# Optimization experiments

Hardware: AMD Instinct MI355X
Metric: run time of the kernel (lower is better)

The kernel has to match this reference:

```python
import jax, jax.numpy as jnp
import numpy as np

NUM_HEADS = 12


def setup_inputs() -> dict:
    key = jax.random.key(0)
    k1, k2, k3 = jax.random.split(key, 3)
    B, N, C = 8, 1024, 768
    x = jax.random.normal(k1, (B, N, C), dtype=jnp.float32)
    qkv_w = jax.random.normal(k2, (3 * C, C), dtype=jnp.float32) * (C ** -0.5)
    proj_w = jax.random.normal(k3, (C, C), dtype=jnp.float32) * (C ** -0.5)
    proj_b = jnp.zeros((C,), dtype=jnp.float32)
    return {"x": x, "qkv_w": qkv_w, "proj_w": proj_w, "proj_b": proj_b, "cur_depth": 9}


def reference(x, qkv_w, proj_w, proj_b, cur_depth):
    B, N, C = x.shape
    H = NUM_HEADS
    hd = C // H
    scale = hd ** -0.5
    # qkv projection (no bias): (B,N,3C) -> (3,B,H,N,hd)
    qkv = (x @ qkv_w.T).reshape(B, N, 3, H, hd).transpose(2, 0, 3, 1, 4)
    q, k, v = qkv[0], qkv[1], qkv[2]
    # full attention scores, materialized as in the original
    attn = jnp.einsum("bhqd,bhkd->bhqk", q, k) * scale  # (B,H,N,N)
    # sigmoid gate from the LAST query row's pre-softmax scores, averaged over heads
    # attn[:, :, -1, :] -> (B,H,N); mean over heads -> (B,N); broadcast to (B,1,1,N)
    mask = jax.nn.sigmoid(attn[:, :, -1, :].mean(axis=1))[:, None, None, :]
    attn = jax.nn.softmax(attn, axis=-1)
    if cur_depth >= 9:
        attn = attn * mask
    out = jnp.einsum("bhqk,bhkd->bhqd", attn, v)  # (B,H,N,hd)
    out = out.transpose(0, 2, 1, 3).reshape(B, N, C)
    out = out @ proj_w.T + proj_b
    return (out, mask)
```

## Files before the change

### kernel.cpp

```cpp
#include <hip/hip_runtime.h>
#include <stdint.h>

typedef __bf16 bf16;
typedef __bf16 bf16x8 __attribute__((ext_vector_type(8)));
typedef float f32x4 __attribute__((ext_vector_type(4)));
typedef float f32x16 __attribute__((ext_vector_type(16)));
typedef uint32_t u32x4 __attribute__((ext_vector_type(4)));

#define DEVI static __device__ __forceinline__

DEVI void async_ld16(void* lds, const void* g) {
  __builtin_amdgcn_global_load_lds(
      (const __attribute__((address_space(1))) void*)(uintptr_t)g,
      (__attribute__((address_space(3))) void*)(uint32_t)(uintptr_t)lds,
      16, 0, 0);
}

DEVI f32x4 vsplat(float v) { f32x4 r; r.x = v; r.y = v; r.z = v; r.w = v; return r; }

__global__ __launch_bounds__(256) void cvt3_kernel(
    const float* __restrict__ x, bf16* __restrict__ xb,
    const float* __restrict__ w1, bf16* __restrict__ w1b,
    const float* __restrict__ w2, bf16* __restrict__ w2b) {
  int i = blockIdx.x * 256 + threadIdx.x;
  const float* src; bf16* dst; int idx;
  if (i < 786432) { src = x; dst = xb; idx = i; }
  else if (i < 786432 + 221184) { src = w1; dst = w1b; idx = i - 786432; }
  else if (i < 786432 + 221184 + 73728) { src = w2; dst = w2b; idx = i - 1007616; }
  else return;
  const float4* p = (const float4*)src + (size_t)idx * 2;
  float4 a = p[0], b = p[1];
  bf16x8 o;
  o[0] = (bf16)a.x; o[1] = (bf16)a.y; o[2] = (bf16)a.z; o[3] = (bf16)a.w;
  o[4] = (bf16)b.x; o[5] = (bf16)b.y; o[6] = (bf16)b.z; o[7] = (bf16)b.w;
  *((bf16x8*)dst + idx) = o;
}

DEVI void gemm_stage(bf16* AsD, bf16* BsD, const bf16* A, const bf16* B,
                     int K, int m0, int n0, int kt, int t, int wbase) {
#pragma unroll
  for (int i = 0; i < 2; i++) {
    int unit = i * 256 + t;
    int row = unit >> 2;
    int su = (unit & 3) ^ ((row >> 1) & 3);
    async_ld16(AsD + (size_t)(i * 256 + wbase) * 8,
               A + (size_t)(m0 + row) * K + kt + su * 8);
    async_ld16(BsD + (size_t)(i * 256 + wbase) * 8,
               B + (size_t)(n0 + row) * K + kt + su * 8);
  }
}

template <int MODE>
__global__ __launch_bounds__(256) void gemm_bt_kernel(
    const bf16* __restrict__ A, const bf16* __restrict__ B, int K, int N,
    int nx, bf16* __restrict__ q_out, bf16* __restrict__ k_out,
    bf16* __restrict__ vt_out, float* __restrict__ f_out,
    const float* __restrict__ bias) {
  __shared__ bf16 As[3][128 * 32];
  __shared__ bf16 Bs[3][128 * 32];
  const int t = threadIdx.x;
  const int lane = t & 63, g = lane >> 4, ql = lane & 15;
  const int w = t >> 6, wr = w >> 1, wc = w & 1;
  const int wbase = __builtin_amdgcn_readfirstlane(t & 192);
  const int bid = blockIdx.x;
  const int xcd = bid & 7, i6 = bid >> 3;
  const int yq = i6 / nx;
  const int m0 = (xcd * 8 + yq) * 128, n0 = (i6 - yq * nx) * 128;
  const int nk = K >> 5;

  f32x4 acc[4][4];
#pragma unroll
  for (int i = 0; i < 4; i++)
#pragma unroll
    for (int j = 0; j < 4; j++) acc[i][j] = vsplat(0.f);

  gemm_stage(As[0], Bs[0], A, B, K, m0, n0, 0, t, wbase);
  gemm_stage(As[1], Bs[1], A, B, K, m0, n0, 32, t, wbase);

  int rd = 0;
  for (int kt2 = 0; kt2 < nk; ++kt2) {
    if (kt2 + 1 < nk)
      asm volatile("s_waitcnt vmcnt(4)\n\ts_barrier" ::: "memory");
    else
      asm volatile("s_waitcnt vmcnt(0)\n\ts_barrier" ::: "memory");
    if (kt2 + 2 < nk) {
      int wb = rd >= 1 ? rd - 1 : 2;
      gemm_stage(As[wb], Bs[wb], A, B, K, m0, n0, (kt2 + 2) * 32, t, wbase);
    }
    const bf16* Asc = As[rd];
    const bf16* Bsc = Bs[rd];
    bf16x8 af[4], bfr[4];
#pragma unroll
    for (int f = 0; f < 4; f++) {
      int ra = wr * 64 + f * 16 + ql;
      af[f] = *(const bf16x8*)(Asc + ra * 32 + ((g ^ ((ra >> 1) & 3)) * 8));
      int rb = wc * 64 + f * 16 + ql;
      bfr[f] = *(const bf16x8*)(Bsc + rb * 32 + ((g ^ ((rb >> 1) & 3)) * 8));
    }
#pragma unroll
    for (int fm = 0; fm < 4; fm++)
#pragma unroll
      for (int fn = 0; fn < 4; fn++)
        acc[fm][fn] = __builtin_amdgcn_mfma_f32_16x16x32_bf16(af[fm], bfr[fn],
                                                              acc[fm][fn], 0, 0, 0);
    rd = rd < 2 ? rd + 1 : 0;
  }

  if (MODE == 0) {
#pragma unroll
    for (int fm = 0; fm < 4; fm++) {
#pragma unroll
      for (int fn = 0; fn < 4; fn++) {
        int n = n0 + wc * 64 + fn * 16 + ql;
#pragma unroll
        for (int r = 0; r < 4; r++) {
          int m = m0 + wr * 64 + fm * 16 + g * 4 + r;
          int b = m >> 10, nn = m & 1023;
          float v = acc[fm][fn][r];
          if (n < 768) {
            int h = n >> 6, d = n & 63;
            q_out[((size_t)((b * 12 + h) * 1024 + nn)) * 64 + d] = (bf16)(v * 0.125f);
          } else if (n < 1536) {
            int c = n - 768, h = c >> 6, d = c & 63;
            k_out[((size_t)((b * 12 + h) * 1024 + nn)) * 64 + d] = (bf16)v;
          } else {
            int c = n - 1536, h = c >> 6, d = c & 63;
            vt_out[((size_t)((b * 12 + h) * 64 + d)) * 1024 + nn] = (bf16)v;
          }
        }
      }
    }
  } else {
#pragma unroll
    for (int fm = 0; fm < 4; fm++) {
#pragma unroll
      for (int fn = 0; fn < 4; fn++) {
        int n = n0 + wc * 64 + fn * 16 + ql;
        float bv = bias[n];
#pragma unroll
        for (int r = 0; r < 4; r++) {
          int m = m0 + wr * 64 + fm * 16 + g * 4 + r;
          f_out[(size_t)m * N + n] = acc[fm][fn][r] + bv;
        }
      }
    }
  }
}

__global__ __launch_bounds__(256) void mask_kernel(
    const bf16* __restrict__ qb, const bf16* __restrict__ kb, float* __restrict__ mout) {
  int t = threadIdx.x, lane = t & 63;
  int wid = blockIdx.x * 4 + (t >> 6);
  int b = wid >> 10, kcol = wid & 1023;
  float acc = 0.f;
#pragma unroll
  for (int h = 0; h < 12; h++) {
    const bf16* qr = qb + ((size_t)((b * 12 + h) * 1024 + 1023)) * 64;
    const bf16* kr = kb + ((size_t)((b * 12 + h) * 1024 + kcol)) * 64;
    acc += (float)qr[lane] * (float)kr[lane];
  }
#pragma unroll
  for (int off = 32; off >= 1; off >>= 1) acc += __shfl_xor(acc, off);
  if (lane == 0) {
    float x = acc * (1.f / 12.f);
    mout[(b << 10) + kcol] = 1.f / (1.f + __expf(-x));
  }
}

__global__ __launch_bounds__(256) void vscale_kernel(
    bf16* __restrict__ vt, const float* __restrict__ maskp, const int* __restrict__ cdp) {
  const bool am = (cdp[0] >= 9);
  int i = blockIdx.x * 256 + threadIdx.x;
  int row = i >> 7, gcol = i & 127;
  size_t off = ((size_t)blockIdx.y * 768 + row) * 1024 + gcol * 8;
  const float* mp = maskp + blockIdx.y * 1024 + gcol * 8;
  float4 m0 = *(const float4*)mp;
  float4 m1 = *(const float4*)(mp + 4);
  float mm[8] = {m0.x, m0.y, m0.z, m0.w, m1.x, m1.y, m1.z, m1.w};
  bf16x8 v = *(bf16x8*)(vt + off);
#pragma unroll
  for (int e = 0; e < 8; e++) {
    float f = am ? mm[e] : 1.0f;
    v[e] = (bf16)((float)v[e] * f);
  }
  *(bf16x8*)(vt + off) = v;
}

DEVI void attn_stage(bf16* KsD, bf16* VsD, const bf16* Kp, const bf16* Vp,
                     int kv0, int t, int wbase) {
#pragma unroll
  for (int i = 0; i < 2; i++) {
    int unit = i * 256 + t;
    int row = unit >> 3;
    int su = (unit & 7) ^ (row & 7);
    async_ld16(KsD + (size_t)(i * 256 + wbase) * 8,
               Kp + (size_t)(kv0 + row) * 64 + su * 8);
    async_ld16(VsD + (size_t)(i * 256 + wbase) * 8,
               Vp + (size_t)row * 1024 + kv0 + su * 8);
  }
}

__global__ __launch_bounds__(256) void attn_kernel(
    const bf16* __restrict__ qb, const bf16* __restrict__ kb,
    const bf16* __restrict__ vt, bf16* __restrict__ ob) {
  __shared__ bf16 Ks[2][64 * 64];
  __shared__ bf16 Vs[2][64 * 64];
  const int t = threadIdx.x;
  const int lane = t & 63, j = lane & 31, hi = lane >> 5;
  const int w = t >> 6;
  const int wbase = __builtin_amdgcn_readfirstlane(t & 192);
  int bid = (blockIdx.x & 7) * 96 + (blockIdx.x >> 3);
  const int bh = bid >> 3, qt = bid & 7;
  const int b = bh / 12, h = bh - b * 12;
  const bf16* Qp = qb + (size_t)bh * 65536;
  const bf16* Kp = kb + (size_t)bh * 65536;
  const bf16* Vp = vt + (size_t)bh * 65536;
  const int q0 = qt * 128 + w * 32;

  bf16x8 qf[4];
#pragma unroll
  for (int ds = 0; ds < 4; ds++)
    qf[ds] = *(const bf16x8*)(Qp + (size_t)(q0 + j) * 64 + hi * 8 + ds * 16);

  f32x16 o0, o1;
#pragma unroll
  for (int i = 0; i < 16; i++) { o0[i] = 0.f; o1[i] = 0.f; }
  float m = -1e30f, D = 0.f;

  attn_stage(Ks[0], Vs[0], Kp, Vp, 0, t, wbase);
  int cur = 0;
  for (int kv0 = 0; kv0 < 1024; kv0 += 64) {
    __syncthreads();
    if (kv0 + 64 < 1024)
      attn_stage(Ks[cur ^ 1], Vs[cur ^ 1], Kp, Vp, kv0 + 64, t, wbase);
    const bf16* Ksc = Ks[cur];
    const bf16* Vsc = Vs[cur];

    f32x16 s0, s1;
#pragma unroll
    for (int i = 0; i < 16; i++) { s0[i] = 0.f; s1[i] = 0.f; }
    __builtin_amdgcn_s_setprio(1);
#pragma unroll
    for (int ds = 0; ds < 4; ds++) {
      int c = hi + 2 * ds;
      bf16x8 k0 = *(const bf16x8*)(Ksc + j * 64 + ((c ^ (j & 7)) * 8));
      s0 = __builtin_amdgcn_mfma_f32_32x32x16_bf16(k0, qf[ds], s0, 0, 0, 0);
      int r1 = 32 + j;
      bf16x8 k1 = *(const bf16x8*)(Ksc + r1 * 64 + ((c ^ (r1 & 7)) * 8));
      s1 = __builtin_amdgcn_mfma_f32_32x32x16_bf16(k1, qf[ds], s1, 0, 0, 0);
    }
    __builtin_amdgcn_s_setprio(0);

    float tm = s0[0];
#pragma unroll
    for (int i = 1; i < 16; i++) tm = fmaxf(tm, s0[i]);
#pragma unroll
    for (int i = 0; i < 16; i++) tm = fmaxf(tm, s1[i]);
    tm = fmaxf(tm, __shfl_xor(tm, 32));
    if (!__all(tm <= m + 8.f)) {
      float mn = fmaxf(m, tm);
      float sc = __expf(m - mn);
      m = mn;
      D *= sc;
#pragma unroll
      for (int i = 0; i < 16; i++) { o0[i] *= sc; o1[i] *= sc; }
    }
#pragma unroll
    for (int i = 0; i < 16; i++) s0[i] = __expf(s0[i] - m);
#pragma unroll
    for (int i = 0; i < 16; i++) s1[i] = __expf(s1[i] - m);
    float rs = 0.f;
#pragma unroll
    for (int i = 0; i < 16; i++) rs += s0[i] + s1[i];
    rs += __shfl_xor(rs, 32);
    D += rs;

    bf16x8 pf[4];
#pragma unroll
    for (int ks = 0; ks < 4; ks++) {
      int base = 8 * (ks & 1);
      float pA0, pA1, pB0, pB1, pA2, pA3, pB2, pB3;
      if (ks & 2) {
        pA0 = s1[base]; pA1 = s1[base + 1]; pB0 = s1[base + 4]; pB1 = s1[base + 5];
        pA2 = s1[base + 2]; pA3 = s1[base + 3]; pB2 = s1[base + 6]; pB3 = s1[base + 7];
      } else {
        pA0 = s0[base]; pA1 = s0[base + 1]; pB0 = s0[base + 4]; pB1 = s0[base + 5];
        pA2 = s0[base + 2]; pA3 = s0[base + 3]; pB2 = s0[base + 6]; pB3 = s0[base + 7];
      }
      uint32_t CA, CB, CA2, CB2;
      asm("v_cvt_pk_bf16_f32 %0, %1, %2" : "=v"(CA) : "v"(pA0), "v"(pA1));
      asm("v_cvt_pk_bf16_f32 %0, %1, %2" : "=v"(CB) : "v"(pB0), "v"(pB1));
      asm("v_permlane32_swap_b32 %0, %1" : "+v"(CA), "+v"(CB));
      asm("v_cvt_pk_bf16_f32 %0, %1, %2" : "=v"(CA2) : "v"(pA2), "v"(pA3));
      asm("v_cvt_pk_bf16_f32 %0, %1, %2" : "=v"(CB2) : "v"(pB2), "v"(pB3));
      asm("v_permlane32_swap_b32 %0, %1" : "+v"(CA2), "+v"(CB2));
      u32x4 dw;
      dw[0] = CA; dw[1] = CA2; dw[2] = CB; dw[3] = CB2;
      pf[ks] = __builtin_bit_cast(bf16x8, dw);
    }

    __builtin_amdgcn_s_setprio(1);
#pragma unroll
    for (int ks = 0; ks < 4; ks++) {
      int c = hi + 2 * ks;
      bf16x8 v0 = *(const bf16x8*)(Vsc + j * 64 + ((c ^ (j & 7)) * 8));
      o0 = __builtin_amdgcn_mfma_f32_32x32x16_bf16(pf[ks], v0, o0, 0, 0, 0);
      int r1 = 32 + j;
      bf16x8 v1 = *(const bf16x8*)(Vsc + r1 * 64 + ((c ^ (r1 & 7)) * 8));
      o1 = __builtin_amdgcn_mfma_f32_32x32x16_bf16(pf[ks], v1, o1, 0, 0, 0);
    }
    __builtin_amdgcn_s_setprio(0);
    cur ^= 1;
  }

  float dinv = 1.f / D;
#pragma unroll
  for (int reg = 0; reg < 16; reg++) {
    int qrow = (reg & 3) + 8 * (reg >> 2) + 4 * hi;
    float dv = __shfl(dinv, qrow);
    bf16* dst = ob + (size_t)(b * 1024 + q0 + qrow) * 768 + h * 64 + j;
    dst[0]  = (bf16)(o0[reg] * dv);
    dst[32] = (bf16)(o1[reg] * dv);
  }
}

extern "C" void kernel_launch(void* const* d_in, const int* in_sizes, int n_in,
                              void* d_out, int out_size, void* d_ws, size_t ws_size,
                              hipStream_t stream) {
  const float* x     = (const float*)d_in[0];
  const float* qkvw  = (const float*)d_in[1];
  const float* projw = (const float*)d_in[2];
  const float* projb = (const float*)d_in[3];
  const int*   cd    = (const int*)d_in[4];
  float* out  = (float*)d_out;
  float* mout = out + 6291456;

  char* p = (char*)d_ws;
  bf16* xb    = (bf16*)p; p += 12582912;
  bf16* wqkvb = (bf16*)p; p += 3538944;
  bf16* wpb   = (bf16*)p; p += 1179648;
  bf16* qb    = (bf16*)p; p += 12582912;
  bf16* kb    = (bf16*)p; p += 12582912;
  bf16* vtb   = (bf16*)p; p += 12582912;
  bf16* obuf  = xb;

  cvt3_kernel<<<4224, 256, 0, stream>>>(x, xb, qkvw, wqkvb, projw, wpb);
  gemm_bt_kernel<0><<<1152, 256, 0, stream>>>(
      xb, wqkvb, 768, 2304, 18, qb, kb, vtb, nullptr, nullptr);
  mask_kernel<<<2048, 256, 0, stream>>>(qb, kb, mout);
  vscale_kernel<<<dim3(384, 8), 256, 0, stream>>>(vtb, mout, cd);
  attn_kernel<<<768, 256, 0, stream>>>(qb, kb, vtb, obuf);
  gemm_bt_kernel<1><<<384, 256, 0, stream>>>(
      obuf, wpb, 768, 768, 6, nullptr, nullptr, nullptr, out, projb);
}
```

Baseline: 214.3 us.

## Enlarge GEMM tiles to 256x128 with K=64 steps and 512-thread blocks

Reworks the bf16 GEMM kernel to use 512-thread blocks computing 256x128 output tiles, with K-step raised from 32 to 64 and an 8-way XOR swizzle for the wider LDS rows. Grid sizes are halved for both the QKV and output projection GEMMs. The aim is more data reuse per LDS load and fewer barrier/loop iterations. In exchange it uses much more LDS per block, allows only one block per CU, and halves the number of blocks, which may cost occupancy on the smaller projection GEMM.

```diff
diff --git a/kernel.cpp b/kernel.cpp
--- a/kernel.cpp
+++ b/kernel.cpp
@@ -39,34 +39,40 @@
 DEVI void gemm_stage(bf16* AsD, bf16* BsD, const bf16* A, const bf16* B,
                      int K, int m0, int n0, int kt, int t, int wbase) {
 #pragma unroll
-  for (int i = 0; i < 2; i++) {
-    int unit = i * 256 + t;
-    int row = unit >> 2;
-    int su = (unit & 3) ^ ((row >> 1) & 3);
-    async_ld16(AsD + (size_t)(i * 256 + wbase) * 8,
+  for (int p = 0; p < 4; p++) {
+    int unit = p * 512 + t;
+    int row = unit >> 3;
+    int su = (unit & 7) ^ (row & 7);
+    async_ld16(AsD + (size_t)(p * 512 + wbase) * 8,
                A + (size_t)(m0 + row) * K + kt + su * 8);
-    async_ld16(BsD + (size_t)(i * 256 + wbase) * 8,
+  }
+#pragma unroll
+  for (int p = 0; p < 2; p++) {
+    int unit = p * 512 + t;
+    int row = unit >> 3;
+    int su = (unit & 7) ^ (row & 7);
+    async_ld16(BsD + (size_t)(p * 512 + wbase) * 8,
                B + (size_t)(n0 + row) * K + kt + su * 8);
   }
 }
 
 template <int MODE>
-__global__ __launch_bounds__(256) void gemm_bt_kernel(
+__global__ __launch_bounds__(512, 1) void gemm_bt_kernel(
     const bf16* __restrict__ A, const bf16* __restrict__ B, int K, int N,
     int nx, bf16* __restrict__ q_out, bf16* __restrict__ k_out,
     bf16* __restrict__ vt_out, float* __restrict__ f_out,
     const float* __restrict__ bias) {
-  __shared__ bf16 As[3][128 * 32];
-  __shared__ bf16 Bs[3][128 * 32];
+  __shared__ bf16 As[3][256 * 64];
+  __shared__ bf16 Bs[3][128 * 64];
   const int t = threadIdx.x;
   const int lane = t & 63, g = lane >> 4, ql = lane & 15;
   const int w = t >> 6, wr = w >> 1, wc = w & 1;
-  const int wbase = __builtin_amdgcn_readfirstlane(t & 192);
+  const int wbase = __builtin_amdgcn_readfirstlane(t & 448);
   const int bid = blockIdx.x;
   const int xcd = bid & 7, i6 = bid >> 3;
   const int yq = i6 / nx;
-  const int m0 = (xcd * 8 + yq) * 128, n0 = (i6 - yq * nx) * 128;
-  const int nk = K >> 5;
+  const int m0 = (xcd * 4 + yq) * 256, n0 = (i6 - yq * nx) * 128;
+  const int nk = K >> 6;
 
   f32x4 acc[4][4];
 #pragma unroll
@@ -75,34 +81,39 @@
     for (int j = 0; j < 4; j++) acc[i][j] = vsplat(0.f);
 
   gemm_stage(As[0], Bs[0], A, B, K, m0, n0, 0, t, wbase);
-  gemm_stage(As[1], Bs[1], A, B, K, m0, n0, 32, t, wbase);
+  gemm_stage(As[1], Bs[1], A, B, K, m0, n0, 64, t, wbase);
 
   int rd = 0;
   for (int kt2 = 0; kt2 < nk; ++kt2) {
     if (kt2 + 1 < nk)
-      asm volatile("s_waitcnt vmcnt(4)\n\ts_barrier" ::: "memory");
+      asm volatile("s_waitcnt vmcnt(6)\n\ts_barrier" ::: "memory");
     else
       asm volatile("s_waitcnt vmcnt(0)\n\ts_barrier" ::: "memory");
     if (kt2 + 2 < nk) {
       int wb = rd >= 1 ? rd - 1 : 2;
-      gemm_stage(As[wb], Bs[wb], A, B, K, m0, n0, (kt2 + 2) * 32, t, wbase);
+      gemm_stage(As[wb], Bs[wb], A, B, K, m0, n0, (kt2 + 2) * 64, t, wbase);
     }
     const bf16* Asc = As[rd];
     const bf16* Bsc = Bs[rd];
-    bf16x8 af[4], bfr[4];
-#pragma unroll
-    for (int f = 0; f < 4; f++) {
-      int ra = wr * 64 + f * 16 + ql;
-      af[f] = *(const bf16x8*)(Asc + ra * 32 + ((g ^ ((ra >> 1) & 3)) * 8));
-      int rb = wc * 64 + f * 16 + ql;
-      bfr[f] = *(const bf16x8*)(Bsc + rb * 32 + ((g ^ ((rb >> 1) & 3)) * 8));
-    }
-#pragma unroll
-    for (int fm = 0; fm < 4; fm++)
-#pragma unroll
-      for (int fn = 0; fn < 4; fn++)
-        acc[fm][fn] = __builtin_amdgcn_mfma_f32_16x16x32_bf16(af[fm], bfr[fn],
-                                                              acc[fm][fn], 0, 0, 0);
+    bf16x8 af[2][4], bfr[2][4];
+#pragma unroll
+    for (int kh = 0; kh < 2; kh++) {
+#pragma unroll
+      for (int f = 0; f < 4; f++) {
+        int ra = wr * 64 + f * 16 + ql;
+        af[kh][f] = *(const bf16x8*)(Asc + ra * 64 + (((kh * 4 + g) ^ (ra & 7)) * 8));
+        int rb = wc * 64 + f * 16 + ql;
+        bfr[kh][f] = *(const bf16x8*)(Bsc + rb * 64 + (((kh * 4 + g) ^ (rb & 7)) * 8));
+      }
+    }
+#pragma unroll
+    for (int kh = 0; kh < 2; kh++)
+#pragma unroll
+      for (int fm = 0; fm < 4; fm++)
+#pragma unroll
+        for (int fn = 0; fn < 4; fn++)
+          acc[fm][fn] = __builtin_amdgcn_mfma_f32_16x16x32_bf16(
+              af[kh][fm], bfr[kh][fn], acc[fm][fn], 0, 0, 0);
     rd = rd < 2 ? rd + 1 : 0;
   }
 
@@ -345,11 +356,11 @@
   bf16* obuf  = xb;
 
   cvt3_kernel<<<4224, 256, 0, stream>>>(x, xb, qkvw, wqkvb, projw, wpb);
-  gemm_bt_kernel<0><<<1152, 256, 0, stream>>>(
+  gemm_bt_kernel<0><<<576, 512, 0, stream>>>(
       xb, wqkvb, 768, 2304, 18, qb, kb, vtb, nullptr, nullptr);
   mask_kernel<<<2048, 256, 0, stream>>>(qb, kb, mout);
   vscale_kernel<<<dim3(384, 8), 256, 0, stream>>>(vtb, mout, cd);
   attn_kernel<<<768, 256, 0, stream>>>(qb, kb, vtb, obuf);
-  gemm_bt_kernel<1><<<384, 256, 0, stream>>>(
+  gemm_bt_kernel<1><<<192, 512, 0, stream>>>(
       obuf, wpb, 768, 768, 6, nullptr, nullptr, nullptr, out, projb);
 }
```

Result: no change. 213.2 us (-0.5%).
